# Kernel optimization log

Measured on AMD Instinct MI355X. Metric: run time of the kernel, lower is better.

## Reference

```python
import jax, jax.numpy as jnp
import numpy as np

BATCH = 128
SPEC_STEPS = 8
VOCAB = 128000


def setup_inputs() -> dict:
    key = jax.random.key(0)
    k1, k2, k3 = jax.random.split(key, 3)
    # Ragged draft counts per request in [1, SPEC_STEPS]
    counts = np.random.default_rng(0).integers(1, SPEC_STEPS + 1, size=BATCH)
    cu = np.cumsum(counts).astype(np.int32)
    num_tokens = int(cu[-1])
    draft_token_ids = jax.random.randint(k1, (num_tokens,), 0, VOCAB, dtype=jnp.int32)
    target_logits = jax.random.normal(k2, (num_tokens, VOCAB), dtype=jnp.float32)
    bonus_token_ids = jax.random.randint(k3, (BATCH,), 0, VOCAB, dtype=jnp.int32)
    return {
        "draft_token_ids": draft_token_ids,
        "num_spec_steps": SPEC_STEPS,
        "cu_num_draft_tokens": jnp.asarray(cu),
        "target_logits": target_logits,
        "bonus_token_ids": bonus_token_ids,
    }


def reference(draft_token_ids, num_spec_steps, cu_num_draft_tokens, target_logits, bonus_token_ids):
    INVALID = jnp.int32(-1)
    S = num_spec_steps  # python int
    # Greedy target token per draft position: [T]
    target_argmax = jnp.argmax(target_logits, axis=-1).astype(jnp.int32)

    starts = jnp.concatenate([jnp.zeros((1,), cu_num_draft_tokens.dtype), cu_num_draft_tokens[:-1]])
    n_draft = (cu_num_draft_tokens - starts).astype(jnp.int32)  # [B]

    pos = jnp.arange(S, dtype=jnp.int32)                 # [S]
    valid = pos[None, :] < n_draft[:, None]              # [B,S] pos < num_draft
    tok_idx = jnp.where(valid, starts[:, None].astype(jnp.int32) + pos[None, :], 0)
    d = draft_token_ids[tok_idx]                         # [B,S]
    t = target_argmax[tok_idx]                           # [B,S]

    mismatch = valid & (d != t)                          # [B,S]
    mi = mismatch.astype(jnp.int32)
    # rejected BEFORE this position (kernel stores argmax at the mismatch pos itself)
    prev_rejected = (jnp.cumsum(mi, axis=1) - mi) > 0    # exclusive prefix any-mismatch
    written = jnp.where(prev_rejected, INVALID, t)       # value stored at pos < num_draft

    rejected = jnp.any(mismatch, axis=1)                 # [B]
    processed = jnp.sum((valid & ~prev_rejected).astype(jnp.int32), axis=1)
    num_bonus_tokens = (processed - 1 + (~rejected).astype(jnp.int32)).astype(jnp.int32)

    bonus_col = jnp.where(rejected, INVALID, bonus_token_ids)  # [B]

    pos2 = jnp.arange(S + 1, dtype=jnp.int32)[None, :]   # [1,S+1]
    written_p = jnp.pad(written, ((0, 0), (0, 1)), constant_values=-1)
    output_token_ids = jnp.where(
        pos2 < n_draft[:, None], written_p,
        jnp.where(pos2 == n_draft[:, None], bonus_col[:, None], INVALID)
    ).astype(jnp.int32)  # [B, S+1]; slots past bonus are -1 (torch version leaves them uninitialized)

    return output_token_ids, num_bonus_tokens
```

## Files before the change

### kernel.cpp

```cpp
#include <hip/hip_runtime.h>
#include <hip/hip_bf16.h>
#include <math.h>


typedef float f32x4 __attribute__((ext_vector_type(4)));

__device__ __forceinline__ void combine(float& bv, int& bi, float v, int i) {
    if (v > bv || (v == bv && i < bi)) { bv = v; bi = i; }
}

template <int BLOCK, int NS>
__global__ void __launch_bounds__(BLOCK)
argmax_partial_kernel(const float* __restrict__ logits, int vocab,
                      float* __restrict__ ws_val, int* __restrict__ ws_idx) {
    const int bid = blockIdx.x;
    const int row = bid / NS;
    const int seg = bid % NS;
    const int seg_len = vocab / NS;
    const int seg_beg = seg * seg_len;
    const int seg_end = (seg == NS - 1) ? vocab : seg_beg + seg_len;

    const float* rowp = logits + (size_t)row * (size_t)vocab;
    const int tid = threadIdx.x;

    float bv = -INFINITY;
    int   bi = 0x7fffffff;

    const int beg4 = seg_beg >> 2;
    const int end4 = seg_end >> 2;
    const f32x4* p4 = (const f32x4*)rowp;
    for (int j = beg4 + tid; j < end4; j += BLOCK) {
        f32x4 v = __builtin_nontemporal_load(&p4[j]);
        const int base = j << 2;
        combine(bv, bi, v.x, base + 0);
        combine(bv, bi, v.y, base + 1);
        combine(bv, bi, v.z, base + 2);
        combine(bv, bi, v.w, base + 3);
    }
    for (int j = (end4 << 2) + tid; j < seg_end; j += BLOCK) {
        combine(bv, bi, rowp[j], j);
    }

    #pragma unroll
    for (int off = 32; off >= 1; off >>= 1) {
        float ov = __shfl_down(bv, off, 64);
        int   oi = __shfl_down(bi, off, 64);
        combine(bv, bi, ov, oi);
    }

    constexpr int NW = BLOCK / 64;
    __shared__ float sv[NW];
    __shared__ int   si[NW];
    const int wave = tid >> 6;
    if ((tid & 63) == 0) { sv[wave] = bv; si[wave] = bi; }
    __syncthreads();
    if (tid == 0) {
        #pragma unroll
        for (int w = 1; w < NW; ++w) combine(bv, bi, sv[w], si[w]);
        ws_val[bid] = bv;
        ws_idx[bid] = bi;
    }
}

template <int NS>
__global__ void finalize_kernel(const int* __restrict__ draft,
                                const int* __restrict__ cu,
                                const float* __restrict__ ws_val,
                                const int* __restrict__ ws_idx,
                                const int* __restrict__ bonus,
                                int* __restrict__ out_tokens,
                                int* __restrict__ out_bonus,
                                int B, int S) {
    const int b = blockIdx.x * blockDim.x + threadIdx.x;
    if (b >= B) return;
    const int start = (b == 0) ? 0 : cu[b - 1];
    const int n     = cu[b] - start;
    int* row = out_tokens + (size_t)b * (S + 1);

    bool rejected  = false;
    int  processed = 0;
    for (int p = 0; p < S + 1; ++p) {
        int val;
        if (p < n) {
            if (!rejected) {
                const int base = (start + p) * NS;
                float bv = -INFINITY;
                int   bi = 0x7fffffff;
                #pragma unroll
                for (int s = 0; s < NS; ++s)
                    combine(bv, bi, ws_val[base + s], ws_idx[base + s]);
                val = bi;
                ++processed;
                if (draft[start + p] != bi) rejected = true;
            } else {
                val = -1;
            }
        } else if (p == n) {
            val = rejected ? -1 : bonus[b];
        } else {
            val = -1;
        }
        row[p] = val;
    }
    out_bonus[b] = processed - 1 + (rejected ? 0 : 1);
}

extern "C" void kernel_launch(void* const* d_in, const int* in_sizes, int n_in,
                              void* d_out, int out_size, void* d_ws, size_t ws_size,
                              hipStream_t stream) {
    const int*   draft  = (const int*)d_in[0];
    const int*   cu     = (const int*)d_in[2];
    const float* logits = (const float*)d_in[3];
    const int*   bonus  = (const int*)d_in[4];

    const int T     = in_sizes[0];
    const int B     = in_sizes[2];
    const int vocab = in_sizes[3] / T;
    const int S     = out_size / B - 2;

    constexpr int NS    = 8;
    constexpr int BLOCK = 256;

    float* ws_val = (float*)d_ws;
    int*   ws_idx = (int*)(ws_val + (size_t)T * NS);
    int* out_tokens = (int*)d_out;
    int* out_bonus  = out_tokens + (size_t)B * (S + 1);

    argmax_partial_kernel<BLOCK, NS><<<T * NS, BLOCK, 0, stream>>>(
        logits, vocab, ws_val, ws_idx);
    finalize_kernel<NS><<<(B + 127) / 128, 128, 0, stream>>>(
        draft, cu, ws_val, ws_idx, bonus, out_tokens, out_bonus, B, S);
}
```

Baseline: 59.21 us.

## Fuse argmax and rejection into one cooperative persistent kernel

Merges the partial-argmax and finalize kernels into a single cooperative kernel with a fixed grid of 1024 blocks that loops over chunks, uses a grid-wide sync, and then performs per-request rejection with parallel per-token reductions. It also splits each row into 16 segments instead of 8 and tracks four independent per-lane maxima to shorten the compare dependency chain. This is meant to remove the second launch and the serial finalize reduction, at the cost of a grid barrier and persistent-loop overhead.

After: 189.9 us. 221% more time.

```diff
diff --git a/kernel.cpp b/kernel.cpp
--- a/kernel.cpp
+++ b/kernel.cpp
@@ -1,6 +1,9 @@
 #include <hip/hip_runtime.h>
 #include <hip/hip_bf16.h>
+#include <hip/hip_cooperative_groups.h>
 #include <math.h>
+
+namespace cg = cooperative_groups;
 
 
 typedef float f32x4 __attribute__((ext_vector_type(4)));
@@ -11,98 +14,111 @@
 
 template <int BLOCK, int NS>
 __global__ void __launch_bounds__(BLOCK)
-argmax_partial_kernel(const float* __restrict__ logits, int vocab,
-                      float* __restrict__ ws_val, int* __restrict__ ws_idx) {
-    const int bid = blockIdx.x;
-    const int row = bid / NS;
-    const int seg = bid % NS;
-    const int seg_len = vocab / NS;
-    const int seg_beg = seg * seg_len;
-    const int seg_end = (seg == NS - 1) ? vocab : seg_beg + seg_len;
-
-    const float* rowp = logits + (size_t)row * (size_t)vocab;
+fused_rejection_kernel(const float* __restrict__ logits, int vocab, int T,
+                       const int* __restrict__ draft,
+                       const int* __restrict__ cu,
+                       const int* __restrict__ bonus,
+                       float* __restrict__ ws_val, int* __restrict__ ws_idx,
+                       int* __restrict__ out_tokens, int* __restrict__ out_bonus,
+                       int B, int S) {
     const int tid = threadIdx.x;
-
-    float bv = -INFINITY;
-    int   bi = 0x7fffffff;
-
-    const int beg4 = seg_beg >> 2;
-    const int end4 = seg_end >> 2;
-    const f32x4* p4 = (const f32x4*)rowp;
-    for (int j = beg4 + tid; j < end4; j += BLOCK) {
-        f32x4 v = __builtin_nontemporal_load(&p4[j]);
-        const int base = j << 2;
-        combine(bv, bi, v.x, base + 0);
-        combine(bv, bi, v.y, base + 1);
-        combine(bv, bi, v.z, base + 2);
-        combine(bv, bi, v.w, base + 3);
-    }
-    for (int j = (end4 << 2) + tid; j < seg_end; j += BLOCK) {
-        combine(bv, bi, rowp[j], j);
-    }
-
-    #pragma unroll
-    for (int off = 32; off >= 1; off >>= 1) {
-        float ov = __shfl_down(bv, off, 64);
-        int   oi = __shfl_down(bi, off, 64);
-        combine(bv, bi, ov, oi);
-    }
-
     constexpr int NW = BLOCK / 64;
     __shared__ float sv[NW];
     __shared__ int   si[NW];
-    const int wave = tid >> 6;
-    if ((tid & 63) == 0) { sv[wave] = bv; si[wave] = bi; }
-    __syncthreads();
-    if (tid == 0) {
+    __shared__ int   tok[32];
+
+    const int seg_len = vocab / NS;
+    const int nchunks = T * NS;
+
+    for (int c = blockIdx.x; c < nchunks; c += gridDim.x) {
+        const int row = c / NS;
+        const int seg = c - row * NS;
+        const int seg_beg = seg * seg_len;
+        const int seg_end = (seg == NS - 1) ? vocab : seg_beg + seg_len;
+        const float* rowp = logits + (size_t)row * (size_t)vocab;
+        const f32x4* p4 = (const f32x4*)rowp;
+        const int beg4 = seg_beg >> 2;
+        const int end4 = seg_end >> 2;
+
+        float bv0 = -INFINITY, bv1 = -INFINITY, bv2 = -INFINITY, bv3 = -INFINITY;
+        int   bj0 = 0, bj1 = 0, bj2 = 0, bj3 = 0;
+        for (int j = beg4 + tid; j < end4; j += BLOCK) {
+            f32x4 v = __builtin_nontemporal_load(&p4[j]);
+            if (v.x > bv0) { bv0 = v.x; bj0 = j; }
+            if (v.y > bv1) { bv1 = v.y; bj1 = j; }
+            if (v.z > bv2) { bv2 = v.z; bj2 = j; }
+            if (v.w > bv3) { bv3 = v.w; bj3 = j; }
+        }
+        float bv = bv0; int bi = (bj0 << 2);
+        combine(bv, bi, bv1, (bj1 << 2) | 1);
+        combine(bv, bi, bv2, (bj2 << 2) | 2);
+        combine(bv, bi, bv3, (bj3 << 2) | 3);
+        for (int j2 = (end4 << 2) + tid; j2 < seg_end; j2 += BLOCK)
+            combine(bv, bi, rowp[j2], j2);
+
         #pragma unroll
-        for (int w = 1; w < NW; ++w) combine(bv, bi, sv[w], si[w]);
-        ws_val[bid] = bv;
-        ws_idx[bid] = bi;
+        for (int off = 32; off >= 1; off >>= 1) {
+            float ov = __shfl_down(bv, off, 64);
+            int   oi = __shfl_down(bi, off, 64);
+            combine(bv, bi, ov, oi);
+        }
+        if ((tid & 63) == 0) { sv[tid >> 6] = bv; si[tid >> 6] = bi; }
+        __syncthreads();
+        if (tid == 0) {
+            #pragma unroll
+            for (int w = 1; w < NW; ++w) combine(bv, bi, sv[w], si[w]);
+            ws_val[c] = bv;
+            ws_idx[c] = bi;
+        }
+        __syncthreads();
     }
-}
 
-template <int NS>
-__global__ void finalize_kernel(const int* __restrict__ draft,
-                                const int* __restrict__ cu,
-                                const float* __restrict__ ws_val,
-                                const int* __restrict__ ws_idx,
-                                const int* __restrict__ bonus,
-                                int* __restrict__ out_tokens,
-                                int* __restrict__ out_bonus,
-                                int B, int S) {
-    const int b = blockIdx.x * blockDim.x + threadIdx.x;
-    if (b >= B) return;
-    const int start = (b == 0) ? 0 : cu[b - 1];
-    const int n     = cu[b] - start;
-    int* row = out_tokens + (size_t)b * (S + 1);
+    cg::this_grid().sync();
 
-    bool rejected  = false;
-    int  processed = 0;
-    for (int p = 0; p < S + 1; ++p) {
-        int val;
-        if (p < n) {
-            if (!rejected) {
-                const int base = (start + p) * NS;
-                float bv = -INFINITY;
-                int   bi = 0x7fffffff;
-                #pragma unroll
-                for (int s = 0; s < NS; ++s)
-                    combine(bv, bi, ws_val[base + s], ws_idx[base + s]);
-                val = bi;
-                ++processed;
-                if (draft[start + p] != bi) rejected = true;
-            } else {
-                val = -1;
+    for (int b = blockIdx.x; b < B; b += gridDim.x) {
+        const int start = (b == 0) ? 0 : cu[b - 1];
+        const int n = cu[b] - start;
+        const int p = tid / NS;
+        const int s = tid % NS;
+        if (p < n && p < 32) {
+            const int c = (start + p) * NS + s;
+            float v = ws_val[c];
+            int   i = ws_idx[c];
+            #pragma unroll
+            for (int off = NS / 2; off >= 1; off >>= 1) {
+                float ov = __shfl_down(v, off, NS);
+                int   oi = __shfl_down(i, off, NS);
+                combine(v, i, ov, oi);
             }
-        } else if (p == n) {
-            val = rejected ? -1 : bonus[b];
-        } else {
-            val = -1;
+            if (s == 0) tok[p] = i;
         }
-        row[p] = val;
+        __syncthreads();
+        if (tid == 0) {
+            int* rowo = out_tokens + (size_t)b * (S + 1);
+            bool rejected = false;
+            int  processed = 0;
+            for (int p2 = 0; p2 <= S; ++p2) {
+                int val;
+                if (p2 < n) {
+                    if (!rejected) {
+                        const int t = tok[p2];
+                        val = t;
+                        ++processed;
+                        if (draft[start + p2] != t) rejected = true;
+                    } else {
+                        val = -1;
+                    }
+                } else if (p2 == n) {
+                    val = rejected ? -1 : bonus[b];
+                } else {
+                    val = -1;
+                }
+                rowo[p2] = val;
+            }
+            out_bonus[b] = processed - 1 + (rejected ? 0 : 1);
+        }
+        __syncthreads();
     }
-    out_bonus[b] = processed - 1 + (rejected ? 0 : 1);
 }
 
 extern "C" void kernel_launch(void* const* d_in, const int* in_sizes, int n_in,
@@ -113,21 +129,27 @@
     const float* logits = (const float*)d_in[3];
     const int*   bonus  = (const int*)d_in[4];
 
-    const int T     = in_sizes[0];
-    const int B     = in_sizes[2];
-    const int vocab = in_sizes[3] / T;
-    const int S     = out_size / B - 2;
+    int T     = in_sizes[0];
+    int B     = in_sizes[2];
+    int vocab = in_sizes[3] / T;
+    int S     = out_size / B - 2;
 
-    constexpr int NS    = 8;
+    constexpr int NS    = 16;
     constexpr int BLOCK = 256;
+    constexpr int GRID  = 1024;
 
     float* ws_val = (float*)d_ws;
     int*   ws_idx = (int*)(ws_val + (size_t)T * NS);
     int* out_tokens = (int*)d_out;
     int* out_bonus  = out_tokens + (size_t)B * (S + 1);
 
-    argmax_partial_kernel<BLOCK, NS><<<T * NS, BLOCK, 0, stream>>>(
-        logits, vocab, ws_val, ws_idx);
-    finalize_kernel<NS><<<(B + 127) / 128, 128, 0, stream>>>(
-        draft, cu, ws_val, ws_idx, bonus, out_tokens, out_bonus, B, S);
+    void* args[] = {
+        (void*)&logits, (void*)&vocab, (void*)&T,
+        (void*)&draft, (void*)&cu, (void*)&bonus,
+        (void*)&ws_val, (void*)&ws_idx,
+        (void*)&out_tokens, (void*)&out_bonus,
+        (void*)&B, (void*)&S,
+    };
+    hipLaunchCooperativeKernel((void*)fused_rejection_kernel<BLOCK, NS>,
+                               dim3(GRID), dim3(BLOCK), args, 0, stream);
 }
```
